# Optimization experiments

Hardware: AMD Instinct MI355X
Metric: run time of the kernel (lower is better)

The kernel has to match this reference:

```python
import jax, jax.numpy as jnp
import numpy as np

BN_EPS = 1e-5


def _gcn_norm(edge_index, n):
    # PyG gcn_norm with add_self_loops=True: deg counts in-degree incl. self loop
    loops = jnp.arange(n, dtype=edge_index.dtype)
    src = jnp.concatenate([edge_index[0], loops])
    dst = jnp.concatenate([edge_index[1], loops])
    deg = jax.ops.segment_sum(jnp.ones(src.shape[0], jnp.float32), dst, num_segments=n)
    dinv = jnp.where(deg > 0, jax.lax.rsqrt(jnp.maximum(deg, 1.0)), 0.0)
    norm = dinv[src] * dinv[dst]  # [E + N]
    return src, dst, norm


def _gcn_conv(x, src, dst, norm, W, b, n):
    h = x @ W                      # dense transform first (fewer FLOPs: d_out gather)
    msgs = h[src] * norm[:, None]  # [E+N, d_out] gathered, degree-normalized
    return jax.ops.segment_sum(msgs, dst, num_segments=n) + b


def _bn_relu(x, gamma, beta):
    # BatchNorm1d in training mode: biased batch stats over node dim
    mu = x.mean(axis=0)
    var = x.var(axis=0)
    return jax.nn.relu(gamma * (x - mu) * jax.lax.rsqrt(var + BN_EPS) + beta)


def setup_inputs() -> dict:
    key = jax.random.key(0)
    ks = jax.random.split(key, 8)
    N, E, D_IN, H1, H2, D_OUT = 50000, 500000, 128, 256, 512, 128
    x = jax.random.normal(ks[0], (N, D_IN), jnp.float32)
    edge_index = jax.random.randint(ks[1], (2, E), 0, N, jnp.int64)
    def lin(k, fan_in, fan_out):
        bound = 1.0 / np.sqrt(fan_in)
        kw, kb = jax.random.split(k)
        W = jax.random.uniform(kw, (fan_in, fan_out), jnp.float32, -bound, bound)
        b = jax.random.uniform(kb, (fan_out,), jnp.float32, -bound, bound)
        return W, b
    W1, b1 = lin(ks[2], D_IN, H1)
    W2, b2 = lin(ks[3], H1, H2)
    Wl, bl = lin(ks[4], H2, D_OUT)
    return {
        "x": x, "edge_index": edge_index,
        "W1": W1, "b1": b1, "gamma1": jnp.ones((H1,), jnp.float32), "beta1": jnp.zeros((H1,), jnp.float32),
        "W2": W2, "b2": b2, "gamma2": jnp.ones((H2,), jnp.float32), "beta2": jnp.zeros((H2,), jnp.float32),
        "Wl": Wl, "bl": bl,
    }


def reference(x, edge_index, W1, b1, gamma1, beta1, W2, b2, gamma2, beta2, Wl, bl):
    n = x.shape[0]
    src, dst, norm = _gcn_norm(edge_index, n)
    h = _bn_relu(_gcn_conv(x, src, dst, norm, W1, b1, n), gamma1, beta1)
    h = _bn_relu(_gcn_conv(h, src, dst, norm, W2, b2, n), gamma2, beta2)
    return h @ Wl + bl
```

## Files before the change

kernel.cpp:

```cpp
#include <hip/hip_runtime.h>
#include <cstdint>
#include <cstddef>

typedef __bf16 bf16;
typedef bf16 bf16x2 __attribute__((ext_vector_type(2)));
typedef bf16 bf16x4 __attribute__((ext_vector_type(4)));
typedef bf16 bf16x8 __attribute__((ext_vector_type(8)));
typedef float f32x4 __attribute__((ext_vector_type(4)));

__device__ __forceinline__ void gll16(const void* g, void* l) {
  __builtin_amdgcn_global_load_lds((__attribute__((address_space(1))) void*)g,
                                   (__attribute__((address_space(3))) void*)l, 16, 0, 0);
}

__global__ void k_init(int* __restrict__ deg, int* __restrict__ cur, int N) {
  int i = blockIdx.x * 256 + threadIdx.x;
  if (i < N) { deg[i] = 1; cur[i] = 0; }
}

__global__ void k_count(const int* __restrict__ ei, int* __restrict__ deg, int E) {
  int e = blockIdx.x * 256 + threadIdx.x;
  if (e < E) atomicAdd(&deg[ei[E + e]], 1);
}

__global__ __launch_bounds__(256) void k_scan1(const int* __restrict__ deg,
                                               int* __restrict__ bsum, int N) {
  int t = threadIdx.x;
  int i = blockIdx.x * 256 + t;
  int v = (i < N) ? deg[i] - 1 : 0;
#pragma unroll
  for (int off = 32; off > 0; off >>= 1) v += __shfl_down(v, off, 64);
  __shared__ int red[4];
  if ((t & 63) == 0) red[t >> 6] = v;
  __syncthreads();
  if (t == 0) bsum[blockIdx.x] = red[0] + red[1] + red[2] + red[3];
}

__global__ __launch_bounds__(256) void k_scan2(const int* __restrict__ bsum,
                                               int* __restrict__ bpre, int B) {
  __shared__ int s[256];
  int t = threadIdx.x;
  int v = (t < B) ? bsum[t] : 0;
  s[t] = v;
  __syncthreads();
  for (int off = 1; off < 256; off <<= 1) {
    int add = (t >= off) ? s[t - off] : 0;
    __syncthreads();
    s[t] += add;
    __syncthreads();
  }
  if (t < B) bpre[t] = s[t] - v;
}

__global__ __launch_bounds__(256) void k_scan3(const int* __restrict__ deg,
                                               const int* __restrict__ bpre,
                                               int* __restrict__ roff,
                                               float* __restrict__ dinv, int N) {
  __shared__ int s[256];
  int t = threadIdx.x;
  int i = blockIdx.x * 256 + t;
  int d = (i < N) ? deg[i] : 1;
  int v = d - 1;
  if (i >= N) v = 0;
  s[t] = v;
  __syncthreads();
  for (int off = 1; off < 256; off <<= 1) {
    int add = (t >= off) ? s[t - off] : 0;
    __syncthreads();
    s[t] += add;
    __syncthreads();
  }
  if (i < N) {
    int base = bpre[blockIdx.x];
    roff[i] = base + s[t] - v;
    dinv[i] = rsqrtf((float)d);
    if (i == N - 1) roff[N] = base + s[t];
  }
}

__global__ void k_scatter(const int* __restrict__ ei, const int* __restrict__ roff,
                          int* __restrict__ cur, int* __restrict__ csr, int E) {
  int e = blockIdx.x * 256 + threadIdx.x;
  if (e >= E) return;
  int d = ei[E + e];
  int p = atomicAdd(&cur[d], 1);
  csr[roff[d] + p] = ei[e];
}

__global__ void k_cvt_x(const float* __restrict__ x, bf16* __restrict__ xb, size_t total) {
  size_t base = ((size_t)blockIdx.x * 256 + threadIdx.x) * 4;
  if (base >= total) return;
  const float4 v = *(const float4*)(x + base);
  bf16x4 o;
  o[0] = (bf16)v.x; o[1] = (bf16)v.y; o[2] = (bf16)v.z; o[3] = (bf16)v.w;
  *(bf16x4*)(xb + base) = o;
}

__global__ void k_cvt_w(const float* __restrict__ W1, const float* __restrict__ W2,
                        const float* __restrict__ Wl, bf16* __restrict__ w1t,
                        bf16* __restrict__ w2t, bf16* __restrict__ wlt) {
  int i = blockIdx.x * 256 + threadIdx.x;
  if (i < 32768) {
    int n = i >> 7, k = i & 127;
    w1t[i] = (bf16)W1[(size_t)k * 256 + n];
  } else if (i < 163840) {
    int j = i - 32768;
    int n = j >> 8, k = j & 255;
    w2t[j] = (bf16)W2[(size_t)k * 512 + n];
  } else {
    int j = i - 163840;
    int n = j >> 9, k = j & 511;
    wlt[j] = (bf16)Wl[(size_t)k * 128 + n];
  }
}

template<int K, int NOUT, bool FINAL>
__global__ __launch_bounds__(256, 4) void k_gemm(const bf16* __restrict__ A,
                                                 const bf16* __restrict__ Bt,
                                                 bf16* __restrict__ outB,
                                                 float* __restrict__ outF,
                                                 const float* __restrict__ bias,
                                                 float* __restrict__ part,
                                                 const float* __restrict__ scA,
                                                 const float* __restrict__ shA,
                                                 int Mreal) {
  constexpr int MT    = FINAL ? 64 : 128;
  constexpr int RPW   = MT / 32;
  constexpr int NSTEP = K / 32;
  constexpr int SB    = MT * 4 + 512;
  constexpr int NAI   = (MT * 4) / 256;
  __shared__ uint4 lds[2 * SB];
  __shared__ float sstm[512];
  __shared__ float scsh[FINAL ? 1024 : 4];

  const int tid = threadIdx.x;
  const int wv = tid >> 6;
  const int lane = tid & 63;
  const int q = lane >> 4, mr = lane & 15;
  const int m0 = blockIdx.y * MT;
  const int n0 = blockIdx.x * 128;
  const int rw = (wv >> 1) * (MT / 2), cw = (wv & 1) * 64;
  const int wslot = wv << 6;
  const int qx = q ^ (mr & 3);

  const bf16* srcA[NAI];
#pragma unroll
  for (int p = 0; p < NAI; ++p) {
    int slot = p * 256 + tid;
    int row = slot >> 2;
    int c = (slot & 3) ^ (row & 3);
    srcA[p] = A + (size_t)(m0 + row) * K + c * 8;
  }
  const bf16* srcB[2];
#pragma unroll
  for (int p = 0; p < 2; ++p) {
    int slot = p * 256 + tid;
    int row = slot >> 2;
    int c = (slot & 3) ^ (row & 3);
    srcB[p] = Bt + (size_t)(n0 + row) * K + c * 8;
  }
  const int cA8 = (((tid & 3) ^ ((tid >> 2) & 3))) * 8;

  auto issue = [&](int t) {
    uint4* bb = lds + (t & 1) * SB;
    if constexpr (!FINAL) {
#pragma unroll
      for (int p = 0; p < NAI; ++p)
        gll16(srcA[p] + t * 32, bb + p * 256 + wslot);
    }
#pragma unroll
    for (int p = 0; p < 2; ++p)
      gll16(srcB[p] + t * 32, bb + MT * 4 + p * 256 + wslot);
  };

  auto xformA = [&](bf16x8 ra, int t) {
    int kb = t * 32 + cA8;
    float4 s0 = *(const float4*)&scsh[kb];
    float4 s1 = *(const float4*)&scsh[kb + 4];
    float4 h0 = *(const float4*)&scsh[512 + kb];
    float4 h1 = *(const float4*)&scsh[512 + kb + 4];
    bf16x8 o;
    o[0] = (bf16)fmaxf(0.f, (float)ra[0] * s0.x + h0.x);
    o[1] = (bf16)fmaxf(0.f, (float)ra[1] * s0.y + h0.y);
    o[2] = (bf16)fmaxf(0.f, (float)ra[2] * s0.z + h0.z);
    o[3] = (bf16)fmaxf(0.f, (float)ra[3] * s0.w + h0.w);
    o[4] = (bf16)fmaxf(0.f, (float)ra[4] * s1.x + h1.x);
    o[5] = (bf16)fmaxf(0.f, (float)ra[5] * s1.y + h1.y);
    o[6] = (bf16)fmaxf(0.f, (float)ra[6] * s1.z + h1.z);
    o[7] = (bf16)fmaxf(0.f, (float)ra[7] * s1.w + h1.w);
    lds[(t & 1) * SB + tid] = *(uint4*)&o;
  };

  f32x4 acc[RPW][4];
#pragma unroll
  for (int r = 0; r < RPW; ++r)
#pragma unroll
    for (int c = 0; c < 4; ++c) acc[r][c] = (f32x4){0.f, 0.f, 0.f, 0.f};

  if constexpr (FINAL) {
    for (int i = tid; i < 1024; i += 256) scsh[i] = (i < 512) ? scA[i] : shA[i - 512];
    issue(0);
    bf16x8 ra0 = *(const bf16x8*)srcA[0];
    __syncthreads();
    xformA(ra0, 0);
    __syncthreads();
  } else {
    issue(0);
    __syncthreads();
  }

#pragma unroll
  for (int t = 0; t < NSTEP; ++t) {
    bf16x8 raN;
    if (t + 1 < NSTEP) {
      issue(t + 1);
      if constexpr (FINAL) raN = *(const bf16x8*)(srcA[0] + (t + 1) * 32);
    }

    const uint4* bb = lds + (t & 1) * SB;
    const bf16x8* bA = (const bf16x8*)bb;
    const bf16x8* bB = (const bf16x8*)(bb + MT * 4);
    bf16x8 bfr[4];
#pragma unroll
    for (int c = 0; c < 4; ++c) {
      int rb = cw + c * 16 + mr;
      bfr[c] = bB[rb * 4 + qx];
    }
#pragma unroll
    for (int r = 0; r < RPW; ++r) {
      int ra = rw + r * 16 + mr;
      bf16x8 af = bA[ra * 4 + qx];
#pragma unroll
      for (int c = 0; c < 4; ++c)
        acc[r][c] = __builtin_amdgcn_mfma_f32_16x16x32_bf16(af, bfr[c], acc[r][c], 0, 0, 0);
    }
    if constexpr (FINAL) {
      if (t + 1 < NSTEP) xformA(raN, t + 1);
    }
    __syncthreads();
  }

  if constexpr (!FINAL) {
    bf16* ot = (bf16*)lds;
#pragma unroll
    for (int c = 0; c < 4; ++c) {
      float s0 = 0.f, s1 = 0.f;
#pragma unroll
      for (int r = 0; r < RPW; ++r) {
#pragma unroll
        for (int i = 0; i < 4; ++i) {
          int rl = rw + r * 16 + q * 4 + i;
          int cl = cw + c * 16 + mr;
          float v = acc[r][c][i];
          ot[rl * 128 + (cl ^ (((rl >> 2) & 3) << 4))] = (bf16)v;
          if (m0 + rl < Mreal) { s0 += v; s1 += v * v; }
        }
      }
      s0 += __shfl_xor(s0, 16, 64); s0 += __shfl_xor(s0, 32, 64);
      s1 += __shfl_xor(s1, 16, 64); s1 += __shfl_xor(s1, 32, 64);
      if (q == 0) {
        sstm[wv * 64 + c * 16 + mr] = s0;
        sstm[256 + wv * 64 + c * 16 + mr] = s1;
      }
    }
    __syncthreads();
    {
      int ssel = tid >> 7, cl = tid & 127;
      int hi = cl >> 6, lo = cl & 63;
      float v = sstm[ssel * 256 + hi * 64 + lo] + sstm[ssel * 256 + (hi + 2) * 64 + lo];
      part[((size_t)ssel * gridDim.y + blockIdx.y) * NOUT + n0 + cl] = v;
    }
#pragma unroll
    for (int p = 0; p < 8; ++p) {
      int rl = p * 16 + (tid >> 4), c8 = tid & 15;
      uint4 v = *(const uint4*)(ot + rl * 128 + ((c8 * 8) ^ (((rl >> 2) & 3) << 4)));
      *(uint4*)(outB + (size_t)(m0 + rl) * NOUT + n0 + c8 * 8) = v;
    }
  } else {
    float* otf = (float*)lds;
#pragma unroll
    for (int h = 0; h < 2; ++h) {
      __syncthreads();
#pragma unroll
      for (int c = 0; c < 4; ++c)
#pragma unroll
        for (int r = 0; r < RPW; ++r)
#pragma unroll
          for (int i = 0; i < 4; ++i) {
            int rl = rw + r * 16 + q * 4 + i;
            if ((rl >> 5) != h) continue;
            int cl = cw + c * 16 + mr;
            otf[(rl - h * 32) * 128 + (cl ^ (((rl >> 2) & 3) << 4))] = acc[r][c][i];
          }
      __syncthreads();
#pragma unroll
      for (int p = 0; p < 4; ++p) {
        int rl = p * 8 + (tid >> 5), c4 = tid & 31;
        int rg = m0 + h * 32 + rl;
        if (rg < Mreal) {
          float4 v = *(const float4*)(otf + rl * 128 + ((c4 * 4) ^ ((((rl + h * 32) >> 2) & 3) << 4)));
          const float4 bv = *(const float4*)(bias + c4 * 4);
          v.x += bv.x; v.y += bv.y; v.z += bv.z; v.w += bv.w;
          *(float4*)(outF + (size_t)rg * 128 + c4 * 4) = v;
        }
      }
    }
  }
}

template<int C, bool BN>
__global__ __launch_bounds__(256) void k_agg(const bf16* __restrict__ h,
                                             bf16* __restrict__ g,
                                             const int* __restrict__ csr,
                                             const int* __restrict__ roff,
                                             const float* __restrict__ dinv,
                                             const float* __restrict__ scale,
                                             const float* __restrict__ shift,
                                             int N) {
  constexpr int VPL = C / 64;
  const int lane = threadIdx.x & 63;
  const int v = (int)(((unsigned)blockIdx.x * 256 + threadIdx.x) >> 6);
  if (v >= N) return;
  float sc[VPL], sh[VPL];
  if constexpr (BN) {
#pragma unroll
    for (int u = 0; u < VPL; ++u) { sc[u] = scale[lane * VPL + u]; sh[u] = shift[lane * VPL + u]; }
  }
  const float dv = dinv[v];
  float acc[VPL];
#pragma unroll
  for (int u = 0; u < VPL; ++u) acc[u] = 0.f;

  auto loadrow = [&](int src, float* o) {
    const bf16* hr = h + (size_t)src * C + lane * VPL;
    if constexpr (VPL == 2) {
      bf16x2 t = *(const bf16x2*)hr;
      o[0] = (float)t[0]; o[1] = (float)t[1];
    } else {
      bf16x4 t = *(const bf16x4*)hr;
#pragma unroll
      for (int u = 0; u < 4; ++u) o[u] = (float)t[u];
    }
  };
  auto addrow = [&](const float* vv, float ww) {
#pragma unroll
    for (int u = 0; u < VPL; ++u) {
      float xx = vv[u];
      if constexpr (BN) xx = fmaxf(0.f, xx * sc[u] + sh[u]);
      acc[u] += ww * xx;
    }
  };

  {
    float vv[VPL];
    loadrow(v, vv);
    addrow(vv, dv);
  }
  const int beg = roff[v], end = roff[v + 1];
  for (int base = beg; base < end; base += 64) {
    int cnt = min(64, end - base);
    int s = 0; float w = 0.f;
    if (lane < cnt) { s = csr[base + lane]; w = dinv[s]; }
    int j = 0;
    for (; j + 4 <= cnt; j += 4) {
      int sa = __shfl(s, j, 64),     sb = __shfl(s, j + 1, 64);
      int sc2 = __shfl(s, j + 2, 64), sd = __shfl(s, j + 3, 64);
      float wa = __shfl(w, j, 64),     wb = __shfl(w, j + 1, 64);
      float wc = __shfl(w, j + 2, 64), wd = __shfl(w, j + 3, 64);
      float va[VPL], vb[VPL], vc[VPL], vd[VPL];
      loadrow(sa, va); loadrow(sb, vb); loadrow(sc2, vc); loadrow(sd, vd);
      addrow(va, wa); addrow(vb, wb); addrow(vc, wc); addrow(vd, wd);
    }
    for (; j < cnt; ++j) {
      int sj = __shfl(s, j, 64);
      float wj = __shfl(w, j, 64);
      float vv[VPL];
      loadrow(sj, vv);
      addrow(vv, wj);
    }
  }

  bf16* gv = g + (size_t)v * C + lane * VPL;
  if constexpr (VPL == 2) {
    bf16x2 o;
    o[0] = (bf16)(acc[0] * dv); o[1] = (bf16)(acc[1] * dv);
    *(bf16x2*)gv = o;
  } else {
    bf16x4 o;
#pragma unroll
    for (int u = 0; u < 4; ++u) o[u] = (bf16)(acc[u] * dv);
    *(bf16x4*)gv = o;
  }
}

__global__ __launch_bounds__(256) void k_bnfinal(const float* __restrict__ part,
                                                 const float* __restrict__ gamma,
                                                 const float* __restrict__ beta,
                                                 float* __restrict__ scale,
                                                 float* __restrict__ shift,
                                                 int C, int GX, float invN) {
  __shared__ float red[2][4][64];
  int t = threadIdx.x;
  int cl = t & 63, seg = t >> 6;
  int c = blockIdx.x * 64 + cl;
  float s0 = 0.f, s1 = 0.f;
  for (int b = seg; b < GX; b += 4) {
    s0 += part[(size_t)b * C + c];
    s1 += part[(size_t)(GX + b) * C + c];
  }
  red[0][seg][cl] = s0; red[1][seg][cl] = s1;
  __syncthreads();
  if (seg == 0) {
    s0 = red[0][0][cl] + red[0][1][cl] + red[0][2][cl] + red[0][3][cl];
    s1 = red[1][0][cl] + red[1][1][cl] + red[1][2][cl] + red[1][3][cl];
    float mu = s0 * invN;
    float var = s1 * invN - mu * mu;
    float is = rsqrtf(var + 1e-5f);
    float scv = gamma[c] * is;
    scale[c] = scv;
    shift[c] = beta[c] - mu * scv;
  }
}

extern "C" void kernel_launch(void* const* d_in, const int* in_sizes, int n_in,
                              void* d_out, int out_size, void* d_ws, size_t ws_size,
                              hipStream_t stream) {
  const float* x   = (const float*)d_in[0];
  const int*   ei  = (const int*)d_in[1];
  const float* W1  = (const float*)d_in[2];
  const float* g1  = (const float*)d_in[4];
  const float* be1 = (const float*)d_in[5];
  const float* W2  = (const float*)d_in[6];
  const float* g2  = (const float*)d_in[8];
  const float* be2 = (const float*)d_in[9];
  const float* Wl  = (const float*)d_in[10];
  const float* bl  = (const float*)d_in[11];
  float* out = (float*)d_out;

  const int N  = in_sizes[0] / 128;
  const int E  = in_sizes[1] / 2;
  const int Mp = ((N + 127) / 128) * 128;
  const int NB = (N + 255) / 256;
  const int GX = Mp / 128;

  char* p = (char*)d_ws;
  auto carve = [&](size_t bytes) { void* r = (void*)p; p += (bytes + 255) & ~(size_t)255; return r; };
  int*   deg   = (int*)carve(sizeof(int) * N);
  int*   cur   = (int*)carve(sizeof(int) * N);
  int*   roff  = (int*)carve(sizeof(int) * (N + 1));
  int*   csr   = (int*)carve(sizeof(int) * E);
  int*   bsum  = (int*)carve(sizeof(int) * 256);
  int*   bpre  = (int*)carve(sizeof(int) * 256);
  float* dinv  = (float*)carve(sizeof(float) * N);
  float* part1 = (float*)carve(sizeof(float) * 2 * (size_t)GX * 256);
  float* part2 = (float*)carve(sizeof(float) * 2 * (size_t)GX * 512);
  float* sc1   = (float*)carve(sizeof(float) * 256);
  float* sh1   = (float*)carve(sizeof(float) * 256);
  float* sc2   = (float*)carve(sizeof(float) * 512);
  float* sh2   = (float*)carve(sizeof(float) * 512);
  bf16*  w1t   = (bf16*)carve(sizeof(bf16) * 256 * 128);
  bf16*  w2t   = (bf16*)carve(sizeof(bf16) * 512 * 256);
  bf16*  wlt   = (bf16*)carve(sizeof(bf16) * 128 * 512);
  bf16*  xb    = (bf16*)carve(sizeof(bf16) * (size_t)Mp * 128);
  bf16*  ax1   = (bf16*)carve(sizeof(bf16) * (size_t)Mp * 128);
  bf16*  t1    = (bf16*)carve(sizeof(bf16) * (size_t)Mp * 256);
  bf16*  ax2   = (bf16*)carve(sizeof(bf16) * (size_t)Mp * 256);
  bf16*  t2    = (bf16*)carve(sizeof(bf16) * (size_t)Mp * 512);
  (void)n_in; (void)out_size; (void)ws_size;

  const int gE = (E + 255) / 256;
  k_init<<<NB, 256, 0, stream>>>(deg, cur, N);
  k_count<<<gE, 256, 0, stream>>>(ei, deg, E);
  k_scan1<<<NB, 256, 0, stream>>>(deg, bsum, N);
  k_scan2<<<1, 256, 0, stream>>>(bsum, bpre, NB);
  k_scan3<<<NB, 256, 0, stream>>>(deg, bpre, roff, dinv, N);
  k_scatter<<<gE, 256, 0, stream>>>(ei, roff, cur, csr, E);

  k_cvt_x<<<(int)(((size_t)N * 128 / 4 + 255) / 256), 256, 0, stream>>>(x, xb, (size_t)N * 128);
  k_cvt_w<<<896, 256, 0, stream>>>(W1, W2, Wl, w1t, w2t, wlt);

  const int gAgg = (N + 3) / 4;
  k_agg<128, false><<<gAgg, 256, 0, stream>>>(xb, ax1, csr, roff, dinv, nullptr, nullptr, N);
  k_gemm<128, 256, false><<<dim3(2, GX), 256, 0, stream>>>(ax1, w1t, t1, nullptr, nullptr, part1, nullptr, nullptr, N);
  k_bnfinal<<<4, 256, 0, stream>>>(part1, g1, be1, sc1, sh1, 256, GX, 1.f / (float)N);

  k_agg<256, true><<<gAgg, 256, 0, stream>>>(t1, ax2, csr, roff, dinv, sc1, sh1, N);
  k_gemm<256, 512, false><<<dim3(4, GX), 256, 0, stream>>>(ax2, w2t, t2, nullptr, nullptr, part2, nullptr, nullptr, N);
  k_bnfinal<<<8, 256, 0, stream>>>(part2, g2, be2, sc2, sh2, 512, GX, 1.f / (float)N);

  k_gemm<512, 128, true><<<dim3(1, Mp / 64), 256, 0, stream>>>(t2, wlt, nullptr, out, bl, nullptr, sc2, sh2, N);
}
```

Baseline: 352.1 us.

## Pack source index with dinv weight in CSR and unroll aggregation by eight

The CSR array now stores each source index together with its precomputed dinv value, so aggregation no longer does a dependent gather of dinv. The aggregation kernel launches one 64-thread block per node instead of four wavefronts per 256-thread block. It also adds an 8-way unrolled gather loop so more row loads are in flight at once. The cost is doubled CSR storage and bandwidth, extra register pressure from the unroll, and a much larger grid of small blocks.

```diff
diff --git a/kernel.cpp b/kernel.cpp
--- a/kernel.cpp
+++ b/kernel.cpp
@@ -79,12 +79,17 @@
 }
 
 __global__ void k_scatter(const int* __restrict__ ei, const int* __restrict__ roff,
-                          int* __restrict__ cur, int* __restrict__ csr, int E) {
+                          int* __restrict__ cur, int2* __restrict__ csr,
+                          const float* __restrict__ dinv, int E) {
   int e = blockIdx.x * 256 + threadIdx.x;
   if (e >= E) return;
   int d = ei[E + e];
+  int sidx = ei[e];
   int p = atomicAdd(&cur[d], 1);
-  csr[roff[d] + p] = ei[e];
+  int2 val;
+  val.x = sidx;
+  val.y = __float_as_int(dinv[sidx]);
+  csr[roff[d] + p] = val;
 }
 
 __global__ void k_cvt_x(const float* __restrict__ x, bf16* __restrict__ xb, size_t total) {
@@ -309,17 +314,17 @@
 }
 
 template<int C, bool BN>
-__global__ __launch_bounds__(256) void k_agg(const bf16* __restrict__ h,
-                                             bf16* __restrict__ g,
-                                             const int* __restrict__ csr,
-                                             const int* __restrict__ roff,
-                                             const float* __restrict__ dinv,
-                                             const float* __restrict__ scale,
-                                             const float* __restrict__ shift,
-                                             int N) {
+__global__ __launch_bounds__(64) void k_agg(const bf16* __restrict__ h,
+                                            bf16* __restrict__ g,
+                                            const int2* __restrict__ csr,
+                                            const int* __restrict__ roff,
+                                            const float* __restrict__ dinv,
+                                            const float* __restrict__ scale,
+                                            const float* __restrict__ shift,
+                                            int N) {
   constexpr int VPL = C / 64;
-  const int lane = threadIdx.x & 63;
-  const int v = (int)(((unsigned)blockIdx.x * 256 + threadIdx.x) >> 6);
+  const int lane = threadIdx.x;
+  const int v = blockIdx.x;
   if (v >= N) return;
   float sc[VPL], sh[VPL];
   if constexpr (BN) {
@@ -360,8 +365,24 @@
   for (int base = beg; base < end; base += 64) {
     int cnt = min(64, end - base);
     int s = 0; float w = 0.f;
-    if (lane < cnt) { s = csr[base + lane]; w = dinv[s]; }
+    if (lane < cnt) {
+      int2 pr = csr[base + lane];
+      s = pr.x; w = __int_as_float(pr.y);
+    }
     int j = 0;
+    for (; j + 8 <= cnt; j += 8) {
+      int ss[8]; float ww[8];
+#pragma unroll
+      for (int k = 0; k < 8; ++k) {
+        ss[k] = __shfl(s, j + k, 64);
+        ww[k] = __shfl(w, j + k, 64);
+      }
+      float vals[8][VPL];
+#pragma unroll
+      for (int k = 0; k < 8; ++k) loadrow(ss[k], vals[k]);
+#pragma unroll
+      for (int k = 0; k < 8; ++k) addrow(vals[k], ww[k]);
+    }
     for (; j + 4 <= cnt; j += 4) {
       int sa = __shfl(s, j, 64),     sb = __shfl(s, j + 1, 64);
       int sc2 = __shfl(s, j + 2, 64), sd = __shfl(s, j + 3, 64);
@@ -448,7 +469,7 @@
   int*   deg   = (int*)carve(sizeof(int) * N);
   int*   cur   = (int*)carve(sizeof(int) * N);
   int*   roff  = (int*)carve(sizeof(int) * (N + 1));
-  int*   csr   = (int*)carve(sizeof(int) * E);
+  int2*  csr   = (int2*)carve(sizeof(int2) * E);
   int*   bsum  = (int*)carve(sizeof(int) * 256);
   int*   bpre  = (int*)carve(sizeof(int) * 256);
   float* dinv  = (float*)carve(sizeof(float) * N);
@@ -474,17 +495,16 @@
   k_scan1<<<NB, 256, 0, stream>>>(deg, bsum, N);
   k_scan2<<<1, 256, 0, stream>>>(bsum, bpre, NB);
   k_scan3<<<NB, 256, 0, stream>>>(deg, bpre, roff, dinv, N);
-  k_scatter<<<gE, 256, 0, stream>>>(ei, roff, cur, csr, E);
+  k_scatter<<<gE, 256, 0, stream>>>(ei, roff, cur, csr, dinv, E);
 
   k_cvt_x<<<(int)(((size_t)N * 128 / 4 + 255) / 256), 256, 0, stream>>>(x, xb, (size_t)N * 128);
   k_cvt_w<<<896, 256, 0, stream>>>(W1, W2, Wl, w1t, w2t, wlt);
 
-  const int gAgg = (N + 3) / 4;
-  k_agg<128, false><<<gAgg, 256, 0, stream>>>(xb, ax1, csr, roff, dinv, nullptr, nullptr, N);
+  k_agg<128, false><<<N, 64, 0, stream>>>(xb, ax1, csr, roff, dinv, nullptr, nullptr, N);
   k_gemm<128, 256, false><<<dim3(2, GX), 256, 0, stream>>>(ax1, w1t, t1, nullptr, nullptr, part1, nullptr, nullptr, N);
   k_bnfinal<<<4, 256, 0, stream>>>(part1, g1, be1, sc1, sh1, 256, GX, 1.f / (float)N);
 
-  k_agg<256, true><<<gAgg, 256, 0, stream>>>(t1, ax2, csr, roff, dinv, sc1, sh1, N);
+  k_agg<256, true><<<N, 64, 0, stream>>>(t1, ax2, csr, roff, dinv, sc1, sh1, N);
   k_gemm<256, 512, false><<<dim3(4, GX), 256, 0, stream>>>(ax2, w2t, t2, nullptr, nullptr, part2, nullptr, nullptr, N);
   k_bnfinal<<<8, 256, 0, stream>>>(part2, g2, be2, sc2, sh2, 512, GX, 1.f / (float)N);
 
```

After: 348.4 us. Within noise of the previous version (-1.0%).
